# Kernel optimization log

Hardware: AMD Instinct MI355X
Metric: run time of the kernel (lower is better)

The kernel has to match this reference:

```python
import jax, jax.numpy as jnp
import numpy as np

N, E, IN = 90000, 540000, 30
H1, H2, H3, H4 = 128, 128, 128, 64

def _glorot(k, i, o):
    return jax.random.normal(k, (i, o), jnp.float32) * np.float32(np.sqrt(2.0 / (i + o)))

def setup_inputs() -> dict:
    key = jax.random.key(0)
    ks = jax.random.split(key, 20)
    inp = {
        'x': jax.random.normal(ks[0], (N, IN), jnp.float32),
        'edge_index': jax.random.randint(ks[1], (2, E), 0, N, dtype=jnp.int32),
    }
    shapes = [(IN, H1), (H1, H2), (H2, H3), (H3, H4)]
    i = 2
    for br in ('s', 't'):
        for li, (din, dout) in enumerate(shapes, start=1):
            inp[f'w{li}{br}'] = _glorot(ks[i], din, dout); i += 1
            inp[f'b{li}{br}'] = jnp.zeros((dout,), jnp.float32)
    return inp

def _mlp(h, w1, b1, w2, b2):
    # Linear -> (Dropout eval = identity) -> ReLU -> Linear
    return jax.nn.relu(h @ w1 + b1) @ w2 + b2

def _gin(h, src, dst, w1, b1, w2, b2):
    # GINConv with eps=0: MLP(x_i + sum_{j->i} x_j)
    agg = jax.ops.segment_sum(h[src], dst, num_segments=N)
    return _mlp(h + agg, w1, b1, w2, b2)

def reference(x, edge_index, w1s, b1s, w2s, b2s, w3s, b3s, w4s, b4s,
              w1t, b1t, w2t, b2t, w3t, b3t, w4t, b4t):
    src, dst = edge_index[0], edge_index[1]
    z_src = _gin(x, src, dst, w1s, b1s, w2s, b2s)       # [N, H2]
    z_src = _gin(z_src, src, dst, w3s, b3s, w4s, b4s)   # [N, H4]
    z_tar = _gin(x, src, dst, w1t, b1t, w2t, b2t)
    z_tar = _gin(z_tar, src, dst, w3t, b3t, w4t, b4t)
    zs = z_src.reshape(-1, 9, H4)  # [G, 9, H4]
    zt = z_tar.reshape(-1, 9, H4)
    adj = jnp.einsum('gik,gjk->gij', zs, zt)  # per-graph 9x9 matmul
    return adj.reshape(-1, 9)  # [N, 9], matches torch.cat along dim 0
```

## Files before the change

### kernel.cpp

```cpp
#include <hip/hip_runtime.h>
#include <hip/hip_bf16.h>


typedef __attribute__((ext_vector_type(8))) short short8;
typedef __attribute__((ext_vector_type(4))) float f32x4;

#define MAXDEG 64

__device__ inline unsigned short f2bf(float f) {
    union { float f; unsigned u; } v; v.f = f;
    unsigned r = v.u + 0x7fffu + ((v.u >> 16) & 1u);
    return (unsigned short)(r >> 16);
}
__device__ inline float bflo(unsigned u) { return __uint_as_float(u << 16); }
__device__ inline float bfhi(unsigned u) { return __uint_as_float(u & 0xffff0000u); }
__device__ inline unsigned packbf(float a, float b) {
    return (unsigned)f2bf(a) | ((unsigned)f2bf(b) << 16);
}

#define W1S_OFF 0
#define W2S_OFF 4096
#define W3S_OFF 20480
#define W4S_OFF 36864
#define W1T_OFF 45056
#define W2T_OFF 49152
#define W3T_OFF 65536
#define W4T_OFF 81920
#define PACK_USHORTS 90112
#define WPACK_BLOCKS 176

__global__ __launch_bounds__(256) void prep_kernel(
    const float* w0, const float* w1, const float* w2, const float* w3,
    const float* w4, const float* w5, const float* w6, const float* w7,
    unsigned short* __restrict__ pack,
    const float* __restrict__ x, float* __restrict__ xpad,
    int* __restrict__ deg, int N)
{
    if (blockIdx.x < WPACK_BLOCKS) {
        if (threadIdx.x >= 64) return;
        const int prefix[9] = {0, 8, 40, 72, 88, 96, 128, 160, 176};
        const int KTa[8] = {1, 4, 4, 4, 1, 4, 4, 4};
        const int KRa[8] = {30, 128, 128, 128, 30, 128, 128, 128};
        const int Ca[8]  = {128, 128, 128, 64, 128, 128, 128, 64};
        const int DOFF[8] = {W1S_OFF, W2S_OFF, W3S_OFF, W4S_OFF,
                             W1T_OFF, W2T_OFF, W3T_OFF, W4T_OFF};
        const float* Ws[8] = {w0, w1, w2, w3, w4, w5, w6, w7};
        int bid = blockIdx.x;
        int mi = 0;
        while (mi < 7 && bid >= prefix[mi + 1]) ++mi;
        int lt = bid - prefix[mi];
        int kt = lt % KTa[mi], ct = lt / KTa[mi];
        const float* W = Ws[mi];
        int l = threadIdx.x;
        int n = ct * 16 + (l & 15);
        for (int j = 0; j < 8; ++j) {
            int k = kt * 32 + (l >> 4) * 8 + j;
            float v = (k < KRa[mi]) ? W[(size_t)k * Ca[mi] + n] : 0.f;
            pack[(size_t)DOFF[mi] + (size_t)lt * 512 + l * 8 + j] = f2bf(v);
        }
    } else {
        int gid = (blockIdx.x - WPACK_BLOCKS) * 256 + threadIdx.x;
        if (gid < N) deg[gid] = 0;
        if (gid >= N * 32) return;
        int n = gid >> 5, f = gid & 31;
        xpad[gid] = (f < 30) ? x[(size_t)n * 30 + f] : 0.f;
    }
}

__global__ __launch_bounds__(256) void bucket_kernel(
    const int* __restrict__ src, const int* __restrict__ dst,
    int* __restrict__ deg, int* __restrict__ colb, int E)
{
    int e = blockIdx.x * 256 + threadIdx.x;
    if (e < E) {
        int d = dst[e];
        int slot = atomicAdd(&deg[d], 1);
        if (slot < MAXDEG) colb[(size_t)d * MAXDEG + slot] = src[e];
    }
}

__global__ __launch_bounds__(256) void gather30_kernel(
    const float* __restrict__ xpad, const int* __restrict__ deg,
    const int* __restrict__ colb, unsigned short* __restrict__ h1, int N)
{
    int gid = blockIdx.x * 256 + threadIdx.x;
    int node = gid >> 3;
    if (node >= N) return;
    int l = gid & 7;
    const float4* base = (const float4*)xpad;
    float4 a = base[(size_t)node * 8 + l];
    const int* col = colb + (size_t)node * MAXDEG;
    int e = min(deg[node], MAXDEG);
    int i = 0;
    for (; i + 4 <= e; i += 4) {
        int s0 = col[i], s1 = col[i + 1], s2 = col[i + 2], s3 = col[i + 3];
        float4 v0 = base[(size_t)s0 * 8 + l];
        float4 v1 = base[(size_t)s1 * 8 + l];
        float4 v2 = base[(size_t)s2 * 8 + l];
        float4 v3 = base[(size_t)s3 * 8 + l];
        a.x += v0.x; a.y += v0.y; a.z += v0.z; a.w += v0.w;
        a.x += v1.x; a.y += v1.y; a.z += v1.z; a.w += v1.w;
        a.x += v2.x; a.y += v2.y; a.z += v2.z; a.w += v2.w;
        a.x += v3.x; a.y += v3.y; a.z += v3.z; a.w += v3.w;
    }
    for (; i + 2 <= e; i += 2) {
        int s0 = col[i], s1 = col[i + 1];
        float4 v0 = base[(size_t)s0 * 8 + l];
        float4 v1 = base[(size_t)s1 * 8 + l];
        a.x += v0.x; a.y += v0.y; a.z += v0.z; a.w += v0.w;
        a.x += v1.x; a.y += v1.y; a.z += v1.z; a.w += v1.w;
    }
    for (; i < e; ++i) {
        float4 v0 = base[(size_t)col[i] * 8 + l];
        a.x += v0.x; a.y += v0.y; a.z += v0.z; a.w += v0.w;
    }
    uint2 o; o.x = packbf(a.x, a.y); o.y = packbf(a.z, a.w);
    ((uint2*)h1)[(size_t)node * 8 + l] = o;
}

__global__ __launch_bounds__(512, 8) void mlp1_kernel(
    const unsigned short* __restrict__ h1, const unsigned short* __restrict__ pack,
    const float* __restrict__ b1s, const float* __restrict__ b2s,
    const float* __restrict__ b1t, const float* __restrict__ b2t,
    unsigned short* __restrict__ z1cat, int N)
{
    __shared__ __align__(16) unsigned short hs[64 * 40];
    __shared__ __align__(16) unsigned short hm[2][64 * 136];
    const int tid = threadIdx.x;
    const int n0blk = blockIdx.x * 64;

    {
        int row = tid >> 3, off = tid & 7;
        int gn = n0blk + row;
        uint2 v = {0u, 0u};
        if (gn < N) v = *(const uint2*)&h1[(size_t)gn * 32 + off * 4];
        *(uint2*)&hs[row * 40 + off * 4] = v;
    }
    __syncthreads();

    const int half = tid >> 8;
    const int ltid = tid & 255;
    const int wv = ltid >> 6, l = ltid & 63, q = l >> 4, m = l & 15;
    const float* B1 = half ? b1t : b1s;
    const float* B2 = half ? b2t : b2s;
    const int w1off = half ? W1T_OFF : W1S_OFF;
    const int w2off = half ? W2T_OFF : W2S_OFF;
    unsigned short* hmb = hm[half];

    {
        short8 a[4];
        #pragma unroll
        for (int nt = 0; nt < 4; ++nt)
            a[nt] = *(const short8*)&hs[(nt * 16 + m) * 40 + q * 8];
        #pragma unroll
        for (int ci = 0; ci < 2; ++ci) {
            int ct = wv * 2 + ci;
            short8 bf = *(const short8*)&pack[w1off + ((size_t)ct * 64 + l) * 8];
            float bias = B1[ct * 16 + m];
            #pragma unroll
            for (int nt = 0; nt < 4; ++nt) {
                f32x4 acc = {0.f, 0.f, 0.f, 0.f};
                acc = __builtin_amdgcn_mfma_f32_16x16x32_bf16(a[nt], bf, acc, 0, 0, 0);
                #pragma unroll
                for (int r = 0; r < 4; ++r) {
                    float v = fmaxf(acc[r] + bias, 0.f);
                    hmb[(nt * 16 + q * 4 + r) * 136 + ct * 16 + m] = f2bf(v);
                }
            }
        }
    }
    __syncthreads();

    f32x4 acc2[4][2];
    #pragma unroll
    for (int nt = 0; nt < 4; ++nt)
        #pragma unroll
        for (int ci = 0; ci < 2; ++ci)
            acc2[nt][ci] = (f32x4){0.f, 0.f, 0.f, 0.f};
    for (int nt = 0; nt < 4; ++nt) {
        short8 a[4];
        #pragma unroll
        for (int kt = 0; kt < 4; ++kt)
            a[kt] = *(const short8*)&hmb[(nt * 16 + m) * 136 + kt * 32 + q * 8];
        #pragma unroll
        for (int ci = 0; ci < 2; ++ci) {
            int ct = wv * 2 + ci;
            #pragma unroll
            for (int kt = 0; kt < 4; ++kt) {
                short8 bf = *(const short8*)&pack[w2off + ((size_t)(ct * 4 + kt) * 64 + l) * 8];
                acc2[nt][ci] = __builtin_amdgcn_mfma_f32_16x16x32_bf16(a[kt], bf, acc2[nt][ci], 0, 0, 0);
            }
        }
    }
    __syncthreads();
    #pragma unroll
    for (int ci = 0; ci < 2; ++ci) {
        int ct = wv * 2 + ci;
        float bias = B2[ct * 16 + m];
        #pragma unroll
        for (int nt = 0; nt < 4; ++nt)
            #pragma unroll
            for (int r = 0; r < 4; ++r)
                hmb[(nt * 16 + q * 4 + r) * 136 + ct * 16 + m] =
                    f2bf(acc2[nt][ci][r] + bias);
    }
    __syncthreads();
    for (int c = tid; c < 2048; c += 512) {
        int row = c >> 5, off = c & 31;
        int gn = n0blk + row;
        if (gn < N) {
            short8 v = *(const short8*)&hm[off >> 4][row * 136 + (off & 15) * 8];
            *(short8*)&z1cat[(size_t)gn * 256 + off * 8] = v;
        }
    }
}

__global__ __launch_bounds__(512, 8) void mlp2_kernel(
    const unsigned short* __restrict__ z1, const int* __restrict__ deg,
    const int* __restrict__ colb, const unsigned short* __restrict__ pack,
    const float* __restrict__ b3s, const float* __restrict__ b4s,
    const float* __restrict__ b3t, const float* __restrict__ b4t,
    float* __restrict__ z2cat, int N)
{
    __shared__ __align__(16) unsigned short hs[32 * 264];
    __shared__ __align__(16) unsigned short hm[32 * 136];
    const int tid = threadIdx.x;
    const int n0blk = blockIdx.x * 32;

    {
        const int g = tid >> 5, l = tid & 31;
        const uint4* base = (const uint4*)z1;
        for (int it = 0; it < 2; ++it) {
            int row = it * 16 + g;
            int gn = n0blk + row;
            float a0 = 0.f, a1 = 0.f, a2 = 0.f, a3 = 0.f;
            float a4 = 0.f, a5 = 0.f, a6 = 0.f, a7 = 0.f;
            if (gn < N) {
                uint4 s = base[(size_t)gn * 32 + l];
                a0 = bflo(s.x); a1 = bfhi(s.x); a2 = bflo(s.y); a3 = bfhi(s.y);
                a4 = bflo(s.z); a5 = bfhi(s.z); a6 = bflo(s.w); a7 = bfhi(s.w);
                const int* col = colb + (size_t)gn * MAXDEG;
                int e = min(deg[gn], MAXDEG);
                int i = 0;
                for (; i + 4 <= e; i += 4) {
                    int s0 = col[i], s1 = col[i + 1], s2 = col[i + 2], s3 = col[i + 3];
                    uint4 v0 = base[(size_t)s0 * 32 + l];
                    uint4 v1 = base[(size_t)s1 * 32 + l];
                    uint4 v2 = base[(size_t)s2 * 32 + l];
                    uint4 v3 = base[(size_t)s3 * 32 + l];
                    a0 += bflo(v0.x); a1 += bfhi(v0.x); a2 += bflo(v0.y); a3 += bfhi(v0.y);
                    a4 += bflo(v0.z); a5 += bfhi(v0.z); a6 += bflo(v0.w); a7 += bfhi(v0.w);
                    a0 += bflo(v1.x); a1 += bfhi(v1.x); a2 += bflo(v1.y); a3 += bfhi(v1.y);
                    a4 += bflo(v1.z); a5 += bfhi(v1.z); a6 += bflo(v1.w); a7 += bfhi(v1.w);
                    a0 += bflo(v2.x); a1 += bfhi(v2.x); a2 += bflo(v2.y); a3 += bfhi(v2.y);
                    a4 += bflo(v2.z); a5 += bfhi(v2.z); a6 += bflo(v2.w); a7 += bfhi(v2.w);
                    a0 += bflo(v3.x); a1 += bfhi(v3.x); a2 += bflo(v3.y); a3 += bfhi(v3.y);
                    a4 += bflo(v3.z); a5 += bfhi(v3.z); a6 += bflo(v3.w); a7 += bfhi(v3.w);
                }
                for (; i + 2 <= e; i += 2) {
                    int s0 = col[i], s1 = col[i + 1];
                    uint4 v0 = base[(size_t)s0 * 32 + l];
                    uint4 v1 = base[(size_t)s1 * 32 + l];
                    a0 += bflo(v0.x); a1 += bfhi(v0.x); a2 += bflo(v0.y); a3 += bfhi(v0.y);
                    a4 += bflo(v0.z); a5 += bfhi(v0.z); a6 += bflo(v0.w); a7 += bfhi(v0.w);
                    a0 += bflo(v1.x); a1 += bfhi(v1.x); a2 += bflo(v1.y); a3 += bfhi(v1.y);
                    a4 += bflo(v1.z); a5 += bfhi(v1.z); a6 += bflo(v1.w); a7 += bfhi(v1.w);
                }
                for (; i < e; ++i) {
                    uint4 v0 = base[(size_t)col[i] * 32 + l];
                    a0 += bflo(v0.x); a1 += bfhi(v0.x); a2 += bflo(v0.y); a3 += bfhi(v0.y);
                    a4 += bflo(v0.z); a5 += bfhi(v0.z); a6 += bflo(v0.w); a7 += bfhi(v0.w);
                }
            }
            short8 st;
            st[0] = (short)f2bf(a0); st[1] = (short)f2bf(a1);
            st[2] = (short)f2bf(a2); st[3] = (short)f2bf(a3);
            st[4] = (short)f2bf(a4); st[5] = (short)f2bf(a5);
            st[6] = (short)f2bf(a6); st[7] = (short)f2bf(a7);
            *(short8*)&hs[row * 264 + l * 8] = st;
        }
    }
    __syncthreads();

    const int wv = tid >> 6, l = tid & 63, q = l >> 4, m = l & 15;

    for (int br = 0; br < 2; ++br) {
        const int w1off = br ? W3T_OFF : W3S_OFF;
        const int w2off = br ? W4T_OFF : W4S_OFF;
        const float* B1 = br ? b3t : b3s;
        const float* B2 = br ? b4t : b4s;
        if (br) __syncthreads();

        #pragma unroll
        for (int ti = 0; ti < 2; ++ti) {
            const int tile = wv * 2 + ti;
            const int ct = tile & 7;
            const int nt = tile >> 3;
            float bias = B1[ct * 16 + m];
            short8 a[4];
            #pragma unroll
            for (int kt = 0; kt < 4; ++kt)
                a[kt] = *(const short8*)&hs[(nt * 16 + m) * 264 + br * 128 + kt * 32 + q * 8];
            f32x4 acc = {0.f, 0.f, 0.f, 0.f};
            #pragma unroll
            for (int kt = 0; kt < 4; ++kt) {
                short8 bf = *(const short8*)&pack[w1off + ((size_t)(ct * 4 + kt) * 64 + l) * 8];
                acc = __builtin_amdgcn_mfma_f32_16x16x32_bf16(a[kt], bf, acc, 0, 0, 0);
            }
            #pragma unroll
            for (int r = 0; r < 4; ++r) {
                float v = fmaxf(acc[r] + bias, 0.f);
                hm[(nt * 16 + q * 4 + r) * 136 + ct * 16 + m] = f2bf(v);
            }
        }
        __syncthreads();

        {
            const int ct = wv & 3;
            const int nt = wv >> 2;
            float bias = B2[ct * 16 + m];
            short8 a[4];
            #pragma unroll
            for (int kt = 0; kt < 4; ++kt)
                a[kt] = *(const short8*)&hm[(nt * 16 + m) * 136 + kt * 32 + q * 8];
            f32x4 acc = {0.f, 0.f, 0.f, 0.f};
            #pragma unroll
            for (int kt = 0; kt < 4; ++kt) {
                short8 bf = *(const short8*)&pack[w2off + ((size_t)(ct * 4 + kt) * 64 + l) * 8];
                acc = __builtin_amdgcn_mfma_f32_16x16x32_bf16(a[kt], bf, acc, 0, 0, 0);
            }
            #pragma unroll
            for (int r = 0; r < 4; ++r) {
                int gn = n0blk + nt * 16 + q * 4 + r;
                if (gn < N)
                    z2cat[(size_t)gn * 128 + br * 64 + ct * 16 + m] = acc[r] + bias;
            }
        }
    }
}

__global__ __launch_bounds__(256) void einsum9_kernel(
    const float* __restrict__ z2cat, float* __restrict__ out, int G)
{
    int g0 = blockIdx.x * 3;
    __shared__ float ss[27][68];
    __shared__ float tt[27][68];
    const int tid = threadIdx.x;
    for (int idx = tid; idx < 27 * 16; idx += 256) {
        int n = idx >> 4, k4 = idx & 15;
        int g = g0 + n / 9;
        if (g < G) {
            size_t row = (size_t)(g * 9 + (n % 9)) * 128;
            float4 a = *(const float4*)&z2cat[row + k4 * 4];
            float4 b = *(const float4*)&z2cat[row + 64 + k4 * 4];
            *(float4*)&ss[n][k4 * 4] = a;
            *(float4*)&tt[n][k4 * 4] = b;
        }
    }
    __syncthreads();
    if (tid < 243) {
        int gl = tid / 81, rem = tid - gl * 81;
        int i = rem / 9, j = rem - i * 9;
        int g = g0 + gl;
        if (g < G) {
            float acc = 0.f;
            #pragma unroll
            for (int k = 0; k < 64; ++k) acc += ss[gl * 9 + i][k] * tt[gl * 9 + j][k];
            out[(size_t)g * 81 + i * 9 + j] = acc;
        }
    }
}

extern "C" void kernel_launch(void* const* d_in, const int* in_sizes, int n_in,
                              void* d_out, int out_size, void* d_ws, size_t ws_size,
                              hipStream_t stream)
{
    const float* x  = (const float*)d_in[0];
    const int*   ei = (const int*)d_in[1];
    const int N_ = in_sizes[0] / 30;
    const int E_ = in_sizes[1] / 2;
    const int* src = ei;
    const int* dst = ei + E_;

    const float* w1s = (const float*)d_in[2];
    const float* b1s = (const float*)d_in[3];
    const float* w2s = (const float*)d_in[4];
    const float* b2s = (const float*)d_in[5];
    const float* w3s = (const float*)d_in[6];
    const float* b3s = (const float*)d_in[7];
    const float* w4s = (const float*)d_in[8];
    const float* b4s = (const float*)d_in[9];
    const float* w1t = (const float*)d_in[10];
    const float* b1t = (const float*)d_in[11];
    const float* w2t = (const float*)d_in[12];
    const float* b2t = (const float*)d_in[13];
    const float* w3t = (const float*)d_in[14];
    const float* b3t = (const float*)d_in[15];
    const float* w4t = (const float*)d_in[16];
    const float* b4t = (const float*)d_in[17];

    int* deg  = (int*)d_ws;
    int* colb = deg + N_;
    size_t int_bytes = ((size_t)N_ * (1 + MAXDEG)) * sizeof(int);
    size_t pb = (int_bytes + 15) & ~(size_t)15;
    unsigned short* packu = (unsigned short*)((char*)d_ws + pb);
    float* xpad = (float*)(packu + PACK_USHORTS);
    unsigned short* h1    = (unsigned short*)(xpad + (size_t)N_ * 32);
    unsigned short* z1cat = h1 + (size_t)N_ * 32;
    float* z2cat = (float*)(z1cat + (size_t)N_ * 256);
    size_t need = pb + (size_t)PACK_USHORTS * 2
                + (size_t)N_ * 32 * 4
                + (size_t)N_ * 32 * 2
                + (size_t)N_ * 256 * 2
                + (size_t)N_ * 128 * 4;
    if (ws_size < need) return;

    const int nbE  = (E_ + 255) / 256;
    const int nb64 = (N_ + 63) / 64;
    const int nb32 = (N_ + 31) / 32;

    prep_kernel<<<WPACK_BLOCKS + (N_ * 32 + 255) / 256, 256, 0, stream>>>(
        w1s, w2s, w3s, w4s, w1t, w2t, w3t, w4t, packu, x, xpad, deg, N_);

    bucket_kernel<<<nbE, 256, 0, stream>>>(src, dst, deg, colb, E_);

    gather30_kernel<<<(N_ * 8 + 255) / 256, 256, 0, stream>>>(
        xpad, deg, colb, h1, N_);

    mlp1_kernel<<<nb64, 512, 0, stream>>>(h1, packu,
        b1s, b2s, b1t, b2t, z1cat, N_);

    mlp2_kernel<<<nb32, 512, 0, stream>>>(z1cat, deg, colb, packu,
        b3s, b4s, b3t, b4t, z2cat, N_);

    {
        int G = N_ / 9;
        einsum9_kernel<<<(G + 2) / 3, 256, 0, stream>>>(z2cat, (float*)d_out, G);
    }
}
```

Baseline: 242.9 us.

## Fuse per-graph einsum into mlp2 kernel using 36-row blocks

The mlp2 kernel now processes 36 nodes (4 complete graphs) per block instead of 32. It writes the second-layer outputs for both branches into shared memory as fp32 and computes the 9x9 per-graph products directly, so the separate einsum kernel and the z2cat round trip through global memory go away. In exchange, shared memory per block grows, MFMA tiles are padded to 48 rows, and some waves idle in the second layer.

```diff
diff --git a/kernel.cpp b/kernel.cpp
--- a/kernel.cpp
+++ b/kernel.cpp
@@ -220,18 +220,20 @@
     const int* __restrict__ colb, const unsigned short* __restrict__ pack,
     const float* __restrict__ b3s, const float* __restrict__ b4s,
     const float* __restrict__ b3t, const float* __restrict__ b4t,
-    float* __restrict__ z2cat, int N)
-{
-    __shared__ __align__(16) unsigned short hs[32 * 264];
-    __shared__ __align__(16) unsigned short hm[32 * 136];
+    float* __restrict__ out, int N, int G)
+{
+    __shared__ __align__(16) unsigned short hs[48 * 264];
+    __shared__ __align__(16) unsigned short hm[48 * 136];
+    float* hsf = (float*)hs;
     const int tid = threadIdx.x;
-    const int n0blk = blockIdx.x * 32;
+    const int n0blk = blockIdx.x * 36;
 
     {
         const int g = tid >> 5, l = tid & 31;
         const uint4* base = (const uint4*)z1;
-        for (int it = 0; it < 2; ++it) {
+        for (int it = 0; it < 3; ++it) {
             int row = it * 16 + g;
+            if (row >= 36) break;
             int gn = n0blk + row;
             float a0 = 0.f, a1 = 0.f, a2 = 0.f, a3 = 0.f;
             float a4 = 0.f, a5 = 0.f, a6 = 0.f, a7 = 0.f;
@@ -292,8 +294,8 @@
         if (br) __syncthreads();
 
         #pragma unroll
-        for (int ti = 0; ti < 2; ++ti) {
-            const int tile = wv * 2 + ti;
+        for (int ti = 0; ti < 3; ++ti) {
+            const int tile = wv * 3 + ti;
             const int ct = tile & 7;
             const int nt = tile >> 3;
             float bias = B1[ct * 16 + m];
@@ -315,57 +317,42 @@
         }
         __syncthreads();
 
-        {
-            const int ct = wv & 3;
-            const int nt = wv >> 2;
-            float bias = B2[ct * 16 + m];
-            short8 a[4];
-            #pragma unroll
-            for (int kt = 0; kt < 4; ++kt)
-                a[kt] = *(const short8*)&hm[(nt * 16 + m) * 136 + kt * 32 + q * 8];
-            f32x4 acc = {0.f, 0.f, 0.f, 0.f};
-            #pragma unroll
-            for (int kt = 0; kt < 4; ++kt) {
-                short8 bf = *(const short8*)&pack[w2off + ((size_t)(ct * 4 + kt) * 64 + l) * 8];
-                acc = __builtin_amdgcn_mfma_f32_16x16x32_bf16(a[kt], bf, acc, 0, 0, 0);
-            }
-            #pragma unroll
-            for (int r = 0; r < 4; ++r) {
-                int gn = n0blk + nt * 16 + q * 4 + r;
-                if (gn < N)
-                    z2cat[(size_t)gn * 128 + br * 64 + ct * 16 + m] = acc[r] + bias;
-            }
-        }
-    }
-}
-
-__global__ __launch_bounds__(256) void einsum9_kernel(
-    const float* __restrict__ z2cat, float* __restrict__ out, int G)
-{
-    int g0 = blockIdx.x * 3;
-    __shared__ float ss[27][68];
-    __shared__ float tt[27][68];
-    const int tid = threadIdx.x;
-    for (int idx = tid; idx < 27 * 16; idx += 256) {
-        int n = idx >> 4, k4 = idx & 15;
-        int g = g0 + n / 9;
-        if (g < G) {
-            size_t row = (size_t)(g * 9 + (n % 9)) * 128;
-            float4 a = *(const float4*)&z2cat[row + k4 * 4];
-            float4 b = *(const float4*)&z2cat[row + 64 + k4 * 4];
-            *(float4*)&ss[n][k4 * 4] = a;
-            *(float4*)&tt[n][k4 * 4] = b;
-        }
-    }
-    __syncthreads();
-    if (tid < 243) {
+        #pragma unroll
+        for (int ti = 0; ti < 2; ++ti) {
+            const int tile = ti * 8 + wv;
+            if (tile < 12) {
+                const int ct = tile & 3;
+                const int nt = tile >> 2;
+                float bias = B2[ct * 16 + m];
+                short8 a[4];
+                #pragma unroll
+                for (int kt = 0; kt < 4; ++kt)
+                    a[kt] = *(const short8*)&hm[(nt * 16 + m) * 136 + kt * 32 + q * 8];
+                f32x4 acc = {0.f, 0.f, 0.f, 0.f};
+                #pragma unroll
+                for (int kt = 0; kt < 4; ++kt) {
+                    short8 bf = *(const short8*)&pack[w2off + ((size_t)(ct * 4 + kt) * 64 + l) * 8];
+                    acc = __builtin_amdgcn_mfma_f32_16x16x32_bf16(a[kt], bf, acc, 0, 0, 0);
+                }
+                #pragma unroll
+                for (int r = 0; r < 4; ++r)
+                    hsf[(nt * 16 + q * 4 + r) * 132 + br * 64 + ct * 16 + m] =
+                        acc[r] + bias;
+            }
+        }
+    }
+    __syncthreads();
+
+    if (tid < 324) {
         int gl = tid / 81, rem = tid - gl * 81;
         int i = rem / 9, j = rem - i * 9;
-        int g = g0 + gl;
+        int g = blockIdx.x * 4 + gl;
         if (g < G) {
+            const float* srow = &hsf[(gl * 9 + i) * 132];
+            const float* trow = &hsf[(gl * 9 + j) * 132 + 64];
             float acc = 0.f;
             #pragma unroll
-            for (int k = 0; k < 64; ++k) acc += ss[gl * 9 + i][k] * tt[gl * 9 + j][k];
+            for (int k = 0; k < 64; ++k) acc += srow[k] * trow[k];
             out[(size_t)g * 81 + i * 9 + j] = acc;
         }
     }
@@ -407,17 +394,15 @@
     float* xpad = (float*)(packu + PACK_USHORTS);
     unsigned short* h1    = (unsigned short*)(xpad + (size_t)N_ * 32);
     unsigned short* z1cat = h1 + (size_t)N_ * 32;
-    float* z2cat = (float*)(z1cat + (size_t)N_ * 256);
     size_t need = pb + (size_t)PACK_USHORTS * 2
                 + (size_t)N_ * 32 * 4
                 + (size_t)N_ * 32 * 2
-                + (size_t)N_ * 256 * 2
-                + (size_t)N_ * 128 * 4;
+                + (size_t)N_ * 256 * 2;
     if (ws_size < need) return;
 
     const int nbE  = (E_ + 255) / 256;
     const int nb64 = (N_ + 63) / 64;
-    const int nb32 = (N_ + 31) / 32;
+    const int nb36 = (N_ + 35) / 36;
 
     prep_kernel<<<WPACK_BLOCKS + (N_ * 32 + 255) / 256, 256, 0, stream>>>(
         w1s, w2s, w3s, w4s, w1t, w2t, w3t, w4t, packu, x, xpad, deg, N_);
@@ -430,11 +415,6 @@
     mlp1_kernel<<<nb64, 512, 0, stream>>>(h1, packu,
         b1s, b2s, b1t, b2t, z1cat, N_);
 
-    mlp2_kernel<<<nb32, 512, 0, stream>>>(z1cat, deg, colb, packu,
-        b3s, b4s, b3t, b4t, z2cat, N_);
-
-    {
-        int G = N_ / 9;
-        einsum9_kernel<<<(G + 2) / 3, 256, 0, stream>>>(z2cat, (float*)d_out, G);
-    }
-}
+    mlp2_kernel<<<nb36, 512, 0, stream>>>(z1cat, deg, colb, packu,
+        b3s, b4s, b3t, b4t, (float*)d_out, N_, N_ / 9);
+}
```

Measured after the change: 237.1 us. -2.4%, faster.
